# Optimization experiments

Measured on AMD Instinct MI355X. Metric: run time of the kernel, lower is better.

Reference implementation:

```python
import jax, jax.numpy as jnp
import numpy as np

B, L, S, H, E = 2, 2048, 2048, 8, 64
EPS = 1e-8


def setup_inputs() -> dict:
    key = jax.random.key(0)
    k1, k2, k3, k4, k5 = jax.random.split(key, 5)
    query = jax.random.normal(k1, (B, L, H, E), jnp.float32)
    key_t = jax.random.normal(k2, (B, S, H, E), jnp.float32)
    value = jax.random.normal(k3, (B, S, H, E), jnp.float32)
    mask_miss_k = jax.random.bernoulli(k4, 0.1, (B, S, 1))
    mask_miss_q = jax.random.bernoulli(k5, 0.1, (B, L, 1))
    # ensure key position 0 is never missing so no softmax row is fully masked
    mask_miss_k = mask_miss_k.at[:, 0, :].set(False)
    pos = jnp.broadcast_to(jnp.arange(L, dtype=jnp.int32)[None, :, None], (B, L, 1))
    return {"query": query, "key": key_t, "value": value,
            "mask_miss_k": mask_miss_k, "mask_miss_q": mask_miss_q,
            "pos": pos, "causal_mask": 1}


def reference(query, key, value, mask_miss_k, mask_miss_q, pos, causal_mask):
    # query: (B,L,H,E)  key/value: (B,S,H,E)  masks: (B,S,1)/(B,L,1) bool  pos: (B,L,1)
    E_ = query.shape[-1]
    scale = 1.0 / np.sqrt(E_)
    neg_inf = jnp.float32(-jnp.inf)

    scores = jnp.einsum('blhe,bshe->bhls', query, key)  # (B,H,L,S)

    if causal_mask:
        p = pos[..., 0]  # (B,L)
        # M[b,i,j] = -inf where p_j > p_i, broadcast over heads
        m_causal = jnp.where(p[:, None, :] > p[:, :, None], neg_inf, 0.0)[:, None, :, :]
        scores = scores + m_causal

    m_k = jnp.where(mask_miss_k[..., 0][:, None, None, :], neg_inf, 0.0)  # (B,1,1,S)
    m_q = jnp.where(mask_miss_q[..., 0][:, None, :, None], neg_inf, 0.0)  # (B,1,L,1)

    att = jax.nn.relu(jax.nn.softmax(scale * (scores + m_k), axis=-1) + m_q)

    # per-row attention entropy (register_entropy=True path)
    entropy = -jnp.sum(att * jnp.log(jnp.clip(att, EPS, None)), axis=-1)  # (B,H,L)
    entropy = jnp.nan_to_num(entropy, nan=0.0)

    # dropout p=0.0 -> identity; nan_to_num as in original
    A = jnp.nan_to_num(att)
    V = jnp.einsum('bhls,bshd->blhd', A, value)  # (B,L,H,E)
    return V, A, entropy
```

## Files before the change

kernel.cpp:

```cpp
#include <hip/hip_runtime.h>

#define B_ 2
#define L_ 2048
#define S_ 2048
#define H_ 8
#define E_ 64
#define VSTRIDE 136
#define NKV 2097152

typedef float f32x4 __attribute__((ext_vector_type(4)));
typedef short s16x8 __attribute__((ext_vector_type(8)));
typedef unsigned int u32;
typedef u32 u32x4 __attribute__((ext_vector_type(4)));
typedef unsigned short u16;
typedef unsigned long long u64;

__device__ __forceinline__ u32 bc(float f){ return __builtin_bit_cast(u32, f); }
__device__ __forceinline__ float exp2g(float x){ return __builtin_amdgcn_exp2f(x); }

__device__ __forceinline__ s16x8 pack8(f32x4 a, f32x4 b){
  union { s16x8 v; u32 w[4]; } r;
  r.w[0] = __builtin_amdgcn_perm(bc(a[1]), bc(a[0]), 0x07060302u);
  r.w[1] = __builtin_amdgcn_perm(bc(a[3]), bc(a[2]), 0x07060302u);
  r.w[2] = __builtin_amdgcn_perm(bc(b[1]), bc(b[0]), 0x07060302u);
  r.w[3] = __builtin_amdgcn_perm(bc(b[3]), bc(b[2]), 0x07060302u);
  return r.v;
}

__launch_bounds__(256)
__global__ void cast_kv_kernel(const float* __restrict__ K, const float* __restrict__ V,
                               u16* __restrict__ Kb, u16* __restrict__ Vb){
  const size_t o = ((size_t)blockIdx.x * 256 + threadIdx.x) * 8;
  f32x4 k0 = *(const f32x4*)(K + o);
  f32x4 k1 = *(const f32x4*)(K + o + 4);
  f32x4 v0 = *(const f32x4*)(V + o);
  f32x4 v1 = *(const f32x4*)(V + o + 4);
  *(s16x8*)(Kb + o) = pack8(k0, k1);
  *(s16x8*)(Vb + o) = pack8(v0, v1);
}

__launch_bounds__(256, 4)
__global__ void attn_kernel(const float* __restrict__ Q,
                            const u16* __restrict__ Kb,
                            const u16* __restrict__ Vb,
                            const int* __restrict__ maskK,
                            const int* __restrict__ maskQ,
                            const int* __restrict__ causal_p,
                            float* __restrict__ outV,
                            float* __restrict__ outA,
                            float* __restrict__ outEnt)
{
  __shared__ __align__(16) u16 vstage[64 * VSTRIDE];
  __shared__ float lsum[4][32];
  __shared__ float tsum[4][32];
  __shared__ float recipS[32];
  __shared__ __align__(8) unsigned char mkb[2048];

  const int tid  = threadIdx.x;
  const int lane = tid & 63;
  const int wv   = tid >> 6;
  const int quad = lane >> 4;
  const int l15  = lane & 15;
  const int permrow = ((l15 >> 2) << 3) | (l15 & 3);

  const int n   = blockIdx.x;
  const int s   = n >> 3;
  const int bh  = ((n & 7) << 1) | (s >> 6);
  const int b   = bh >> 3;
  const int h   = bh & 7;
  const int iA  = (s & 63) << 4;
  const int iB  = 2032 - iA;

  const int causal = causal_p[0] != 0;
  const int imaxA  = causal ? (iA + 15) : (S_ - 1);
  const int imaxB  = causal ? (iB + 15) : (S_ - 1);
  const int nsup   = (imaxB >> 7) + 1;

  {
    const int* mk = maskK + b * S_ + tid * 8;
    u32 w0 = (u32)(mk[0]!=0) | ((u32)(mk[1]!=0)<<8) | ((u32)(mk[2]!=0)<<16) | ((u32)(mk[3]!=0)<<24);
    u32 w1 = (u32)(mk[4]!=0) | ((u32)(mk[5]!=0)<<8) | ((u32)(mk[6]!=0)<<16) | ((u32)(mk[7]!=0)<<24);
    ((uint2*)mkb)[tid] = make_uint2(w0, w1);
  }

  float* const outArowA = outA + ((size_t)bh * L_ + iA) * S_;
  float* const outArowB = outA + ((size_t)bh * L_ + iB) * S_;

  if (causal){
    const f32x4 z4 = {0.f, 0.f, 0.f, 0.f};
    const int jzA = ((imaxA >> 5) + 1) << 5;
    for (int r = 0; r < 16; ++r)
      for (int c = jzA + (tid << 2); c < S_; c += 1024)
        *(f32x4*)(outArowA + (size_t)r * S_ + c) = z4;
    const int jzB = ((imaxB >> 5) + 1) << 5;
    for (int r = 0; r < 16; ++r)
      for (int c = jzB + (tid << 2); c < S_; c += 1024)
        *(f32x4*)(outArowB + (size_t)r * S_ + c) = z4;
  }

  s16x8 qfA0, qfA1, qfB0, qfB1;
  {
    const float qs = 0.125f * 1.44269504f;
    const float* qa = Q + (((size_t)(b * L_ + iA + l15)) * H_ + h) * E_;
    const float* qb = Q + (((size_t)(b * L_ + iB + l15)) * H_ + h) * E_;
    qfA0 = pack8(*(const f32x4*)(qa + quad*8) * qs,      *(const f32x4*)(qa + quad*8 + 4) * qs);
    qfA1 = pack8(*(const f32x4*)(qa + 32 + quad*8) * qs, *(const f32x4*)(qa + 32 + quad*8 + 4) * qs);
    qfB0 = pack8(*(const f32x4*)(qb + quad*8) * qs,      *(const f32x4*)(qb + quad*8 + 4) * qs);
    qfB1 = pack8(*(const f32x4*)(qb + 32 + quad*8) * qs, *(const f32x4*)(qb + 32 + quad*8 + 4) * qs);
  }

  const int rstride = H_ * E_;
  const u16* const Kbh = Kb + ((size_t)(b * S_) * H_ + h) * E_;
  const u16* const Vbh = Vb + ((size_t)(b * S_) * H_ + h) * E_;
  const f32x4 zero4 = {0.f, 0.f, 0.f, 0.f};
  const int irowA = iA + l15;
  const int irowB = iB + l15;

  __syncthreads();

  float lA = 0.f, tA = 0.f, lB = 0.f, tB = 0.f;
  for (int c = wv; (c << 5) <= imaxB; c += 4){
    const int j0c = c << 5;
    const u16* krow = Kbh + (size_t)(j0c + permrow) * rstride + quad * 8;
    const s16x8 ka0 = *(const s16x8*)(krow);
    const s16x8 ka1 = *(const s16x8*)(krow + 32);
    const s16x8 kb0 = *(const s16x8*)(krow + 4 * rstride);
    const s16x8 kb1 = *(const s16x8*)(krow + 4 * rstride + 32);
    const int jbase = j0c + (quad << 3);
    const u64 mk8 = *(const u64*)(mkb + jbase);
    const u32 mlo = (u32)mk8;
    const u32 mhi = (u32)(mk8 >> 32);
    {
      f32x4 sa = __builtin_amdgcn_mfma_f32_16x16x32_bf16(ka0, qfB0, zero4, 0, 0, 0);
      sa       = __builtin_amdgcn_mfma_f32_16x16x32_bf16(ka1, qfB1, sa, 0, 0, 0);
      f32x4 sb = __builtin_amdgcn_mfma_f32_16x16x32_bf16(kb0, qfB0, zero4, 0, 0, 0);
      sb       = __builtin_amdgcn_mfma_f32_16x16x32_bf16(kb1, qfB1, sb, 0, 0, 0);
      const int rel = irowB - jbase;
      #pragma unroll
      for (int r = 0; r < 4; ++r){
        const bool da = (((mlo >> (8*r)) & 0xffu) != 0u) || (causal && (r > rel));
        const float ea = da ? 0.f : exp2g(sa[r]);
        lB += ea; tB = __builtin_fmaf(ea, sa[r], tB);
        const bool db = (((mhi >> (8*r)) & 0xffu) != 0u) || (causal && (r + 4 > rel));
        const float eb = db ? 0.f : exp2g(sb[r]);
        lB += eb; tB = __builtin_fmaf(eb, sb[r], tB);
      }
    }
    if (j0c <= imaxA){
      f32x4 sa = __builtin_amdgcn_mfma_f32_16x16x32_bf16(ka0, qfA0, zero4, 0, 0, 0);
      sa       = __builtin_amdgcn_mfma_f32_16x16x32_bf16(ka1, qfA1, sa, 0, 0, 0);
      f32x4 sb = __builtin_amdgcn_mfma_f32_16x16x32_bf16(kb0, qfA0, zero4, 0, 0, 0);
      sb       = __builtin_amdgcn_mfma_f32_16x16x32_bf16(kb1, qfA1, sb, 0, 0, 0);
      const int rel = irowA - jbase;
      #pragma unroll
      for (int r = 0; r < 4; ++r){
        const bool da = (((mlo >> (8*r)) & 0xffu) != 0u) || (causal && (r > rel));
        const float ea = da ? 0.f : exp2g(sa[r]);
        lA += ea; tA = __builtin_fmaf(ea, sa[r], tA);
        const bool db = (((mhi >> (8*r)) & 0xffu) != 0u) || (causal && (r + 4 > rel));
        const float eb = db ? 0.f : exp2g(sb[r]);
        lA += eb; tA = __builtin_fmaf(eb, sb[r], tA);
      }
    }
  }

  #pragma unroll
  for (int off = 16; off < 64; off <<= 1){
    lA += __shfl_xor(lA, off);  tA += __shfl_xor(tA, off);
    lB += __shfl_xor(lB, off);  tB += __shfl_xor(tB, off);
  }
  if (lane < 16){
    lsum[wv][l15]      = lA;  tsum[wv][l15]      = tA;
    lsum[wv][16 + l15] = lB;  tsum[wv][16 + l15] = tB;
  }
  __syncthreads();
  if (tid < 32){
    float l = lsum[0][tid] + lsum[1][tid] + lsum[2][tid] + lsum[3][tid];
    float t = (tsum[0][tid] + tsum[1][tid] + tsum[2][tid] + tsum[3][tid]) * 0.69314718f;
    const int i0t = (tid < 16) ? iA : iB;
    const int row = i0t + (tid & 15);
    int qm = maskQ[b * L_ + row];
    float rc  = (qm != 0) ? 0.f : (1.f / l);
    float ent = (qm != 0) ? 0.f : (__logf(l) - t / l);
    recipS[tid] = rc;
    outEnt[(size_t)bh * L_ + row] = ent;
  }
  __syncthreads();

  const float rqA = recipS[l15];
  const float rqB = recipS[16 + l15];

  f32x4 uaccA[4], uaccB[4];
  #pragma unroll
  for (int et = 0; et < 4; ++et){ uaccA[et] = (f32x4)0.f; uaccB[et] = (f32x4)0.f; }

  for (int sp = 0; sp < nsup; ++sp){
    const int j0c = (sp << 7) + (wv << 5);
    if (j0c > imaxB) break;

    {
      const int jp = tid >> 2;
      const int a  = tid & 3;
      const int e0 = a << 4;
      const u16* v0p = Vbh + (size_t)((sp << 7) + 2 * jp) * rstride + e0;
      const u16* v1p = v0p + rstride;
      u32x4 xa = *(const u32x4*)(v0p);
      u32x4 xb = *(const u32x4*)(v0p + 8);
      u32x4 ya = *(const u32x4*)(v1p);
      u32x4 yb = *(const u32x4*)(v1p + 8);
      const int colsw = ((((jp >> 2) + (a << 2)) & 15) << 2) | (jp & 3);
      u32* vsw = (u32*)vstage;
      #pragma unroll
      for (int m = 0; m < 4; ++m){
        vsw[(e0 + 2*m        ) * (VSTRIDE/2) + colsw] = __builtin_amdgcn_perm(ya[m], xa[m], 0x05040100u);
        vsw[(e0 + 2*m + 1    ) * (VSTRIDE/2) + colsw] = __builtin_amdgcn_perm(ya[m], xa[m], 0x07060302u);
        vsw[(e0 + 8 + 2*m    ) * (VSTRIDE/2) + colsw] = __builtin_amdgcn_perm(yb[m], xb[m], 0x05040100u);
        vsw[(e0 + 8 + 2*m + 1) * (VSTRIDE/2) + colsw] = __builtin_amdgcn_perm(yb[m], xb[m], 0x07060302u);
      }
    }

    const u16* krow = Kbh + (size_t)(j0c + permrow) * rstride + quad * 8;
    const s16x8 ka0 = *(const s16x8*)(krow);
    const s16x8 ka1 = *(const s16x8*)(krow + 32);
    const s16x8 kb0 = *(const s16x8*)(krow + 4 * rstride);
    const s16x8 kb1 = *(const s16x8*)(krow + 4 * rstride + 32);
    const int jbase = j0c + (quad << 3);
    const u64 mk8 = *(const u64*)(mkb + jbase);
    const u32 mlo = (u32)mk8;
    const u32 mhi = (u32)(mk8 >> 32);

    {
      f32x4 sa = __builtin_amdgcn_mfma_f32_16x16x32_bf16(ka0, qfB0, zero4, 0, 0, 0);
      sa       = __builtin_amdgcn_mfma_f32_16x16x32_bf16(ka1, qfB1, sa, 0, 0, 0);
      f32x4 sb = __builtin_amdgcn_mfma_f32_16x16x32_bf16(kb0, qfB0, zero4, 0, 0, 0);
      sb       = __builtin_amdgcn_mfma_f32_16x16x32_bf16(kb1, qfB1, sb, 0, 0, 0);
      const int rel = irowB - jbase;
      f32x4 ea, eb;
      #pragma unroll
      for (int r = 0; r < 4; ++r){
        const bool da = (((mlo >> (8*r)) & 0xffu) != 0u) || (causal && (r > rel));
        ea[r] = da ? 0.f : exp2g(sa[r]);
        const bool db = (((mhi >> (8*r)) & 0xffu) != 0u) || (causal && (r + 4 > rel));
        eb[r] = db ? 0.f : exp2g(sb[r]);
      }
      *(f32x4*)(outArowB + (size_t)l15 * S_ + jbase)     = ea * rqB;
      *(f32x4*)(outArowB + (size_t)l15 * S_ + jbase + 4) = eb * rqB;
      const s16x8 pf = pack8(ea, eb);
      #pragma unroll
      for (int et = 0; et < 4; ++et){
        const int gq = ((wv << 2) + quad + (et << 2)) & 15;
        const s16x8 vf = *(const s16x8*)(vstage + (et * 16 + l15) * VSTRIDE + gq * 8);
        uaccB[et] = __builtin_amdgcn_mfma_f32_16x16x32_bf16(pf, vf, uaccB[et], 0, 0, 0);
      }
    }

    if (j0c <= imaxA){
      f32x4 sa = __builtin_amdgcn_mfma_f32_16x16x32_bf16(ka0, qfA0, zero4, 0, 0, 0);
      sa       = __builtin_amdgcn_mfma_f32_16x16x32_bf16(ka1, qfA1, sa, 0, 0, 0);
      f32x4 sb = __builtin_amdgcn_mfma_f32_16x16x32_bf16(kb0, qfA0, zero4, 0, 0, 0);
      sb       = __builtin_amdgcn_mfma_f32_16x16x32_bf16(kb1, qfA1, sb, 0, 0, 0);
      const int rel = irowA - jbase;
      f32x4 ea, eb;
      #pragma unroll
      for (int r = 0; r < 4; ++r){
        const bool da = (((mlo >> (8*r)) & 0xffu) != 0u) || (causal && (r > rel));
        ea[r] = da ? 0.f : exp2g(sa[r]);
        const bool db = (((mhi >> (8*r)) & 0xffu) != 0u) || (causal && (r + 4 > rel));
        eb[r] = db ? 0.f : exp2g(sb[r]);
      }
      *(f32x4*)(outArowA + (size_t)l15 * S_ + jbase)     = ea * rqA;
      *(f32x4*)(outArowA + (size_t)l15 * S_ + jbase + 4) = eb * rqA;
      const s16x8 pf = pack8(ea, eb);
      #pragma unroll
      for (int et = 0; et < 4; ++et){
        const int gq = ((wv << 2) + quad + (et << 2)) & 15;
        const s16x8 vf = *(const s16x8*)(vstage + (et * 16 + l15) * VSTRIDE + gq * 8);
        uaccA[et] = __builtin_amdgcn_mfma_f32_16x16x32_bf16(pf, vf, uaccA[et], 0, 0, 0);
      }
    }
  }

  float* Ubuf = (float*)vstage;
  __syncthreads();
  #pragma unroll
  for (int et = 0; et < 4; ++et)
    #pragma unroll
    for (int r = 0; r < 4; ++r)
      Ubuf[(wv * 16 + (quad << 2) + r) * 64 + et * 16 + l15] = uaccA[et][r];
  __syncthreads();
  {
    const int i  = tid >> 4;
    const int e4 = (tid & 15) << 2;
    f32x4 s0 = *(const f32x4*)(Ubuf + (0 * 16 + i) * 64 + e4);
    f32x4 s1 = *(const f32x4*)(Ubuf + (1 * 16 + i) * 64 + e4);
    f32x4 s2 = *(const f32x4*)(Ubuf + (2 * 16 + i) * 64 + e4);
    f32x4 s3 = *(const f32x4*)(Ubuf + (3 * 16 + i) * 64 + e4);
    f32x4 vout = (s0 + s1 + s2 + s3) * recipS[i];
    *(f32x4*)(outV + (((size_t)(b * L_ + iA + i)) * H_ + h) * E_ + e4) = vout;
  }
  __syncthreads();
  #pragma unroll
  for (int et = 0; et < 4; ++et)
    #pragma unroll
    for (int r = 0; r < 4; ++r)
      Ubuf[(wv * 16 + (quad << 2) + r) * 64 + et * 16 + l15] = uaccB[et][r];
  __syncthreads();
  {
    const int i  = tid >> 4;
    const int e4 = (tid & 15) << 2;
    f32x4 s0 = *(const f32x4*)(Ubuf + (0 * 16 + i) * 64 + e4);
    f32x4 s1 = *(const f32x4*)(Ubuf + (1 * 16 + i) * 64 + e4);
    f32x4 s2 = *(const f32x4*)(Ubuf + (2 * 16 + i) * 64 + e4);
    f32x4 s3 = *(const f32x4*)(Ubuf + (3 * 16 + i) * 64 + e4);
    f32x4 vout = (s0 + s1 + s2 + s3) * recipS[16 + i];
    *(f32x4*)(outV + (((size_t)(b * L_ + iB + i)) * H_ + h) * E_ + e4) = vout;
  }
}

extern "C" void kernel_launch(void* const* d_in, const int* in_sizes, int n_in,
                              void* d_out, int out_size, void* d_ws, size_t ws_size,
                              hipStream_t stream){
  const float* Q  = (const float*)d_in[0];
  const float* K  = (const float*)d_in[1];
  const float* V  = (const float*)d_in[2];
  const int* mk   = (const int*)d_in[3];
  const int* mq   = (const int*)d_in[4];
  const int* cm   = (const int*)d_in[6];

  float* outV   = (float*)d_out;
  float* outA   = outV + (size_t)B_ * L_ * H_ * E_;
  float* outEnt = outA + (size_t)B_ * H_ * L_ * S_;

  u16* Kb = (u16*)d_ws;
  u16* Vb = Kb + NKV;

  cast_kv_kernel<<<dim3(NKV / (256 * 8)), 256, 0, stream>>>(K, V, Kb, Vb);
  attn_kernel<<<dim3(1024), 256, 0, stream>>>(Q, Kb, Vb, mk, mq, cm, outV, outA, outEnt);
}
```

Measured before the change: 346.5 us.

## Pre-transpose V into bf16 [bh][e][s] layout and load V fragments directly

New measurement: 362.3 us. 4.6% more time.

```diff
diff --git a/kernel.cpp b/kernel.cpp
--- a/kernel.cpp
+++ b/kernel.cpp
@@ -5,7 +5,6 @@
 #define S_ 2048
 #define H_ 8
 #define E_ 64
-#define VSTRIDE 136
 #define NKV 2097152
 
 typedef float f32x4 __attribute__((ext_vector_type(4)));
@@ -28,21 +27,53 @@
 }
 
 __launch_bounds__(256)
-__global__ void cast_kv_kernel(const float* __restrict__ K, const float* __restrict__ V,
-                               u16* __restrict__ Kb, u16* __restrict__ Vb){
+__global__ void cast_k_kernel(const float* __restrict__ K, u16* __restrict__ Kb){
   const size_t o = ((size_t)blockIdx.x * 256 + threadIdx.x) * 8;
   f32x4 k0 = *(const f32x4*)(K + o);
   f32x4 k1 = *(const f32x4*)(K + o + 4);
-  f32x4 v0 = *(const f32x4*)(V + o);
-  f32x4 v1 = *(const f32x4*)(V + o + 4);
   *(s16x8*)(Kb + o) = pack8(k0, k1);
-  *(s16x8*)(Vb + o) = pack8(v0, v1);
+}
+
+__launch_bounds__(256)
+__global__ void transpose_v_kernel(const float* __restrict__ V, u16* __restrict__ Vt){
+  __shared__ u32 lds[64 * 68];
+  const int t   = threadIdx.x;
+  const int blk = blockIdx.x;
+  const int bh  = blk >> 4;
+  const int b   = bh >> 3;
+  const int h   = bh & 7;
+  const int s0  = (blk & 15) << 7;
+  {
+    const int jsp = t & 63;
+    const int e0  = (t >> 6) << 4;
+    const float* v0 = V + (((size_t)(b * S_ + s0 + 2 * jsp)) * H_ + h) * E_ + e0;
+    const float* v1 = v0 + H_ * E_;
+    #pragma unroll
+    for (int m = 0; m < 4; ++m){
+      f32x4 x = *(const f32x4*)(v0 + m * 4);
+      f32x4 y = *(const f32x4*)(v1 + m * 4);
+      #pragma unroll
+      for (int k = 0; k < 4; ++k)
+        lds[(e0 + m * 4 + k) * 68 + jsp] = __builtin_amdgcn_perm(bc(y[k]), bc(x[k]), 0x07060302u);
+    }
+  }
+  __syncthreads();
+  {
+    const int e  = t >> 2;
+    const int sg = t & 3;
+    u16* dst = Vt + ((size_t)bh * 64 + e) * (size_t)S_ + s0 + (sg << 5);
+    #pragma unroll
+    for (int m = 0; m < 4; ++m){
+      u32x4 w = *(const u32x4*)(lds + e * 68 + (sg << 4) + m * 4);
+      *(u32x4*)(dst + m * 8) = w;
+    }
+  }
 }
 
 __launch_bounds__(256, 4)
 __global__ void attn_kernel(const float* __restrict__ Q,
                             const u16* __restrict__ Kb,
-                            const u16* __restrict__ Vb,
+                            const u16* __restrict__ Vt,
                             const int* __restrict__ maskK,
                             const int* __restrict__ maskQ,
                             const int* __restrict__ causal_p,
@@ -50,7 +81,7 @@
                             float* __restrict__ outA,
                             float* __restrict__ outEnt)
 {
-  __shared__ __align__(16) u16 vstage[64 * VSTRIDE];
+  __shared__ __align__(16) float Ubuf[64 * 68];
   __shared__ float lsum[4][32];
   __shared__ float tsum[4][32];
   __shared__ float recipS[32];
@@ -110,8 +141,8 @@
   }
 
   const int rstride = H_ * E_;
-  const u16* const Kbh = Kb + ((size_t)(b * S_) * H_ + h) * E_;
-  const u16* const Vbh = Vb + ((size_t)(b * S_) * H_ + h) * E_;
+  const u16* const Kbh  = Kb + ((size_t)(b * S_) * H_ + h) * E_;
+  const u16* const Vtbh = Vt + (size_t)bh * 64 * (size_t)S_;
   const f32x4 zero4 = {0.f, 0.f, 0.f, 0.f};
   const int irowA = iA + l15;
   const int irowB = iB + l15;
@@ -198,32 +229,16 @@
     const int j0c = (sp << 7) + (wv << 5);
     if (j0c > imaxB) break;
 
-    {
-      const int jp = tid >> 2;
-      const int a  = tid & 3;
-      const int e0 = a << 4;
-      const u16* v0p = Vbh + (size_t)((sp << 7) + 2 * jp) * rstride + e0;
-      const u16* v1p = v0p + rstride;
-      u32x4 xa = *(const u32x4*)(v0p);
-      u32x4 xb = *(const u32x4*)(v0p + 8);
-      u32x4 ya = *(const u32x4*)(v1p);
-      u32x4 yb = *(const u32x4*)(v1p + 8);
-      const int colsw = ((((jp >> 2) + (a << 2)) & 15) << 2) | (jp & 3);
-      u32* vsw = (u32*)vstage;
-      #pragma unroll
-      for (int m = 0; m < 4; ++m){
-        vsw[(e0 + 2*m        ) * (VSTRIDE/2) + colsw] = __builtin_amdgcn_perm(ya[m], xa[m], 0x05040100u);
-        vsw[(e0 + 2*m + 1    ) * (VSTRIDE/2) + colsw] = __builtin_amdgcn_perm(ya[m], xa[m], 0x07060302u);
-        vsw[(e0 + 8 + 2*m    ) * (VSTRIDE/2) + colsw] = __builtin_amdgcn_perm(yb[m], xb[m], 0x05040100u);
-        vsw[(e0 + 8 + 2*m + 1) * (VSTRIDE/2) + colsw] = __builtin_amdgcn_perm(yb[m], xb[m], 0x07060302u);
-      }
-    }
-
     const u16* krow = Kbh + (size_t)(j0c + permrow) * rstride + quad * 8;
     const s16x8 ka0 = *(const s16x8*)(krow);
     const s16x8 ka1 = *(const s16x8*)(krow + 32);
     const s16x8 kb0 = *(const s16x8*)(krow + 4 * rstride);
     const s16x8 kb1 = *(const s16x8*)(krow + 4 * rstride + 32);
+    s16x8 vf[4];
+    #pragma unroll
+    for (int et = 0; et < 4; ++et)
+      vf[et] = *(const s16x8*)(Vtbh + (size_t)((et << 4) + l15) * S_ + j0c + (quad << 3));
+
     const int jbase = j0c + (quad << 3);
     const u64 mk8 = *(const u64*)(mkb + jbase);
     const u32 mlo = (u32)mk8;
@@ -247,11 +262,8 @@
       *(f32x4*)(outArowB + (size_t)l15 * S_ + jbase + 4) = eb * rqB;
       const s16x8 pf = pack8(ea, eb);
       #pragma unroll
-      for (int et = 0; et < 4; ++et){
-        const int gq = ((wv << 2) + quad + (et << 2)) & 15;
-        const s16x8 vf = *(const s16x8*)(vstage + (et * 16 + l15) * VSTRIDE + gq * 8);
-        uaccB[et] = __builtin_amdgcn_mfma_f32_16x16x32_bf16(pf, vf, uaccB[et], 0, 0, 0);
-      }
+      for (int et = 0; et < 4; ++et)
+        uaccB[et] = __builtin_amdgcn_mfma_f32_16x16x32_bf16(pf, vf[et], uaccB[et], 0, 0, 0);
     }
 
     if (j0c <= imaxA){
@@ -272,29 +284,25 @@
       *(f32x4*)(outArowA + (size_t)l15 * S_ + jbase + 4) = eb * rqA;
       const s16x8 pf = pack8(ea, eb);
       #pragma unroll
-      for (int et = 0; et < 4; ++et){
-        const int gq = ((wv << 2) + quad + (et << 2)) & 15;
-        const s16x8 vf = *(const s16x8*)(vstage + (et * 16 + l15) * VSTRIDE + gq * 8);
-        uaccA[et] = __builtin_amdgcn_mfma_f32_16x16x32_bf16(pf, vf, uaccA[et], 0, 0, 0);
-      }
-    }
-  }
-
-  float* Ubuf = (float*)vstage;
+      for (int et = 0; et < 4; ++et)
+        uaccA[et] = __builtin_amdgcn_mfma_f32_16x16x32_bf16(pf, vf[et], uaccA[et], 0, 0, 0);
+    }
+  }
+
   __syncthreads();
   #pragma unroll
   for (int et = 0; et < 4; ++et)
     #pragma unroll
     for (int r = 0; r < 4; ++r)
-      Ubuf[(wv * 16 + (quad << 2) + r) * 64 + et * 16 + l15] = uaccA[et][r];
+      Ubuf[(wv * 16 + (quad << 2) + r) * 68 + et * 16 + l15] = uaccA[et][r];
   __syncthreads();
   {
     const int i  = tid >> 4;
     const int e4 = (tid & 15) << 2;
-    f32x4 s0 = *(const f32x4*)(Ubuf + (0 * 16 + i) * 64 + e4);
-    f32x4 s1 = *(const f32x4*)(Ubuf + (1 * 16 + i) * 64 + e4);
-    f32x4 s2 = *(const f32x4*)(Ubuf + (2 * 16 + i) * 64 + e4);
-    f32x4 s3 = *(const f32x4*)(Ubuf + (3 * 16 + i) * 64 + e4);
+    f32x4 s0 = *(const f32x4*)(Ubuf + (0 * 16 + i) * 68 + e4);
+    f32x4 s1 = *(const f32x4*)(Ubuf + (1 * 16 + i) * 68 + e4);
+    f32x4 s2 = *(const f32x4*)(Ubuf + (2 * 16 + i) * 68 + e4);
+    f32x4 s3 = *(const f32x4*)(Ubuf + (3 * 16 + i) * 68 + e4);
     f32x4 vout = (s0 + s1 + s2 + s3) * recipS[i];
     *(f32x4*)(outV + (((size_t)(b * L_ + iA + i)) * H_ + h) * E_ + e4) = vout;
   }
@@ -303,15 +311,15 @@
   for (int et = 0; et < 4; ++et)
     #pragma unroll
     for (int r = 0; r < 4; ++r)
-      Ubuf[(wv * 16 + (quad << 2) + r) * 64 + et * 16 + l15] = uaccB[et][r];
+      Ubuf[(wv * 16 + (quad << 2) + r) * 68 + et * 16 + l15] = uaccB[et][r];
   __syncthreads();
   {
     const int i  = tid >> 4;
     const int e4 = (tid & 15) << 2;
-    f32x4 s0 = *(const f32x4*)(Ubuf + (0 * 16 + i) * 64 + e4);
-    f32x4 s1 = *(const f32x4*)(Ubuf + (1 * 16 + i) * 64 + e4);
-    f32x4 s2 = *(const f32x4*)(Ubuf + (2 * 16 + i) * 64 + e4);
-    f32x4 s3 = *(const f32x4*)(Ubuf + (3 * 16 + i) * 64 + e4);
+    f32x4 s0 = *(const f32x4*)(Ubuf + (0 * 16 + i) * 68 + e4);
+    f32x4 s1 = *(const f32x4*)(Ubuf + (1 * 16 + i) * 68 + e4);
+    f32x4 s2 = *(const f32x4*)(Ubuf + (2 * 16 + i) * 68 + e4);
+    f32x4 s3 = *(const f32x4*)(Ubuf + (3 * 16 + i) * 68 + e4);
     f32x4 vout = (s0 + s1 + s2 + s3) * recipS[16 + i];
     *(f32x4*)(outV + (((size_t)(b * L_ + iB + i)) * H_ + h) * E_ + e4) = vout;
   }
@@ -332,8 +340,9 @@
   float* outEnt = outA + (size_t)B_ * H_ * L_ * S_;
 
   u16* Kb = (u16*)d_ws;
-  u16* Vb = Kb + NKV;
-
-  cast_kv_kernel<<<dim3(NKV / (256 * 8)), 256, 0, stream>>>(K, V, Kb, Vb);
-  attn_kernel<<<dim3(1024), 256, 0, stream>>>(Q, Kb, Vb, mk, mq, cm, outV, outA, outEnt);
-}
+  u16* Vt = Kb + NKV;
+
+  cast_k_kernel<<<dim3(NKV / (256 * 8)), 256, 0, stream>>>(K, Kb);
+  transpose_v_kernel<<<dim3(256), 256, 0, stream>>>(V, Vt);
+  attn_kernel<<<dim3(1024), 256, 0, stream>>>(Q, Kb, Vt, mk, mq, cm, outV, outA, outEnt);
+}
```
